# Optimization experiments

Hardware: AMD Instinct MI355X
Metric: run time of the kernel (lower is better)

The kernel has to match this reference:

```python
import jax, jax.numpy as jnp
import numpy as np

B, T, C, H = 4, 2048, 1024, 16
D = C // H  # head_dim = 64


def setup_inputs() -> dict:
    key = jax.random.key(0)
    ks = jax.random.split(key, 4)
    scale = 1.0 / np.sqrt(C)
    return {
        "x": jax.random.normal(ks[0], (B, T, C), dtype=jnp.float32),
        "attn_mask": jnp.ones((B, T), dtype=jnp.int32),
        "W_qkv": jax.random.normal(ks[1], (C, 3 * C), dtype=jnp.float32) * scale,
        "b_qkv": jnp.zeros((3 * C,), dtype=jnp.float32),
        "W_proj": jax.random.normal(ks[2], (C, C), dtype=jnp.float32) * scale,
        "b_proj": jnp.zeros((C,), dtype=jnp.float32),
    }


def reference(x, attn_mask, W_qkv, b_qkv, W_proj, b_proj):
    b, t, c = x.shape
    qkv = x @ W_qkv + b_qkv                      # (B,T,3C)
    q, k, v = jnp.split(qkv, 3, axis=-1)
    # b t (h d) -> b h t d
    q = q.reshape(b, t, H, D).transpose(0, 2, 1, 3)
    k = k.reshape(b, t, H, D).transpose(0, 2, 1, 3)
    v = v.reshape(b, t, H, D).transpose(0, 2, 1, 3)
    att = jnp.einsum("bhtd,bhsd->bhts", q, k) / jnp.sqrt(jnp.float32(D))
    causal = jnp.tril(jnp.ones((t, t), dtype=bool))[None, None]       # (1,1,T,T)
    pad = (attn_mask[:, None, None, :t] != 0)                         # (B,1,1,T)
    att = jnp.where(causal & pad, att, -jnp.inf)
    att = jax.nn.softmax(att, axis=-1)
    y = jnp.einsum("bhts,bhsd->bhtd", att, v)   # (B,H,T,D)
    y = y.transpose(0, 2, 1, 3).reshape(b, t, c)
    return y @ W_proj + b_proj
```

## Files before the change

### kernel.cpp

```cpp
#include <hip/hip_runtime.h>
#include <math.h>

#define B_ 4
#define T_ 2048
#define C_ 1024
#define H_ 16
#define D_ 64
#define M_ (B_*T_)
#define N1_ (3*C_)

typedef __attribute__((ext_vector_type(8))) short bf16x8;
typedef __attribute__((ext_vector_type(4))) short bf16x4;
typedef __attribute__((ext_vector_type(4))) float f32x4;
typedef __attribute__((ext_vector_type(16))) float f32x16;

__device__ __forceinline__ short f2bf(float f){
  union { float f; unsigned u; } v; v.f = f;
  unsigned r = (v.u + 0x7fffu + ((v.u >> 16) & 1u)) >> 16;
  return (short)r;
}

__device__ __forceinline__ unsigned cvtpk(float lo, float hi){
  unsigned r;
  asm("v_cvt_pk_bf16_f32 %0, %1, %2" : "=v"(r) : "v"(lo), "v"(hi));
  return r;
}

__device__ __forceinline__ void plswap(unsigned &a, unsigned &b){
  asm volatile("v_permlane32_swap_b32 %0, %1" : "+v"(a), "+v"(b));
}
__device__ __forceinline__ float xhalf_add(float x){
  unsigned a = __float_as_uint(x), b = a;
  asm volatile("v_permlane32_swap_b32 %0, %1" : "+v"(a), "+v"(b));
  return __uint_as_float(a) + __uint_as_float(b);
}

__device__ __forceinline__ void gll16(const void* g, void* l){
  __builtin_amdgcn_global_load_lds((const __attribute__((address_space(1))) void*)g,
                                   (__attribute__((address_space(3))) void*)l, 16, 0, 0);
}

__global__ __launch_bounds__(256) void convx(const float* __restrict__ x, short* __restrict__ xb, int n){
  int i = (blockIdx.x*256 + threadIdx.x)*8;
  if (i >= n) return;
  float4 a = *(const float4*)(x+i), b = *(const float4*)(x+i+4);
  bf16x8 o;
  o[0]=f2bf(a.x); o[1]=f2bf(a.y); o[2]=f2bf(a.z); o[3]=f2bf(a.w);
  o[4]=f2bf(b.x); o[5]=f2bf(b.y); o[6]=f2bf(b.z); o[7]=f2bf(b.w);
  *(bf16x8*)(xb+i) = o;
}

__global__ __launch_bounds__(256) void transw(const float* __restrict__ W, short* __restrict__ Wt, int K, int N){
  __shared__ float tl[64][72];
  int tid = threadIdx.x;
  int n0 = blockIdx.x*64, k0 = blockIdx.y*64;
  #pragma unroll
  for (int i=0;i<4;i++){
    int row = (tid>>4) + i*16;
    int col4 = (tid&15)*4;
    float4 v = *(const float4*)&W[(size_t)(k0+row)*N + n0 + col4];
    *(float4*)&tl[row][col4] = v;
  }
  __syncthreads();
  #pragma unroll
  for (int i=0;i<2;i++){
    int nr = (tid>>3) + i*32;
    int ch = tid&7;
    bf16x8 o;
    #pragma unroll
    for (int e=0;e<8;e++) o[e] = f2bf(tl[ch*8+e][nr]);
    *(bf16x8*)&Wt[(size_t)(n0+nr)*K + k0 + ch*8] = o;
  }
}

__global__ __launch_bounds__(512) void gemm256(const short* __restrict__ A, const short* __restrict__ Bt,
           const float* __restrict__ bias, short* __restrict__ outb, int M, int N, int K)
{
  __shared__ __attribute__((aligned(128))) char LDSC[131072];
  const int tid = threadIdx.x;
  const int wv = tid>>6, ln = tid&63;
  const int lnr = ln&15, lg = ln>>4;
  const int wm = wv>>2, wn = wv&3;
  const int nx = gridDim.x;
  const int nwg = nx*gridDim.y;
  const int lin = blockIdx.x + nx*blockIdx.y;
  const int swz = (lin&7)*(nwg>>3) + (lin>>3);
  const int m0 = (swz/nx)*256, n0 = (swz%nx)*256;

  const int sr = tid>>3;
  const int sg = (tid&7) ^ (sr&7);
  const short* Ag = A  + (size_t)(m0 + sr)*K + sg*8;
  const short* Bg = Bt + (size_t)(n0 + sr)*K + sg*8;
  const int wv8 = wv*1024;

  const int fsw = (lg ^ (lnr&7))<<4;
  const int aln = (wm*128 + lnr)*128 + fsw;
  const int bln = (wn*64  + lnr)*128 + fsw;

  auto STAGE = [&](int kt, int bi){
    const short* a = Ag + kt*64;
    const short* b = Bg + kt*64;
    char* ab = LDSC + bi*32768 + wv8;
    char* bb = LDSC + 65536 + bi*32768 + wv8;
    gll16(a,                 ab);
    gll16(a + (size_t)64*K,  ab + 8192);
    gll16(a + (size_t)128*K, ab + 16384);
    gll16(a + (size_t)192*K, ab + 24576);
    gll16(b,                 bb);
    gll16(b + (size_t)64*K,  bb + 8192);
    gll16(b + (size_t)128*K, bb + 16384);
    gll16(b + (size_t)192*K, bb + 24576);
  };

  f32x4 acc[8][4];
  #pragma unroll
  for (int i=0;i<8;i++)
    #pragma unroll
    for (int j=0;j<4;j++) acc[i][j] = (f32x4){0.f,0.f,0.f,0.f};

  const int NT = K >> 6;
  STAGE(0, 0);
  asm volatile("s_waitcnt vmcnt(0)" ::: "memory");
  __builtin_amdgcn_sched_barrier(0);
  __builtin_amdgcn_s_barrier();
  __builtin_amdgcn_sched_barrier(0);

  #pragma unroll 1
  for (int kt = 0; kt < NT; kt++){
    const int cb = kt & 1;
    if (kt + 1 < NT) STAGE(kt + 1, cb ^ 1);

    const char* ab = LDSC + cb*32768;
    const char* bb = LDSC + 65536 + cb*32768;
    #pragma unroll
    for (int ks=0; ks<2; ks++){
      bf16x8 af[8], bfr[4];
      #pragma unroll
      for (int mi=0;mi<8;mi++) af[mi]  = *(const bf16x8*)(ab + ((aln + mi*2048) ^ (ks<<6)));
      #pragma unroll
      for (int ni=0;ni<4;ni++) bfr[ni] = *(const bf16x8*)(bb + ((bln + ni*2048) ^ (ks<<6)));
      __builtin_amdgcn_s_setprio(1);
      #pragma unroll
      for (int mi=0;mi<8;mi++)
        #pragma unroll
        for (int ni=0;ni<4;ni++)
          acc[mi][ni] = __builtin_amdgcn_mfma_f32_16x16x32_bf16(af[mi], bfr[ni], acc[mi][ni], 0,0,0);
      __builtin_amdgcn_s_setprio(0);
    }

    __builtin_amdgcn_sched_barrier(0);
    asm volatile("s_waitcnt vmcnt(0)" ::: "memory");
    __builtin_amdgcn_sched_barrier(0);
    __builtin_amdgcn_s_barrier();
    __builtin_amdgcn_sched_barrier(0);
  }

  #pragma unroll
  for (int mi=0;mi<8;mi++){
    #pragma unroll
    for (int ni=0;ni<4;ni++){
      int col = n0 + wn*64 + ni*16 + lnr;
      float bv = bias[col];
      #pragma unroll
      for (int r=0;r<4;r++){
        int row = m0 + wm*128 + mi*16 + lg*4 + r;
        float v = acc[mi][ni][r] + bv;
        if (col < C_) v *= 0.18033688f;
        outb[(size_t)row*N + col] = f2bf(v);
      }
    }
  }
}

__global__ __launch_bounds__(512) void gemm_proj(const short* __restrict__ A, const short* __restrict__ Bt,
           const float* __restrict__ bias, float* __restrict__ outf, int M, int N, int K)
{
  __shared__ __attribute__((aligned(128))) char LDSC[147456];
  const int tid = threadIdx.x;
  const int wv = tid>>6, ln = tid&63;
  const int lnr = ln&15, lg = ln>>4;
  const int wm = wv>>1, wn = wv&1;
  const int nx = gridDim.x;
  const int nwg = nx*gridDim.y;
  const int lin = blockIdx.x + nx*blockIdx.y;
  const int swz = (lin&7)*(nwg>>3) + (lin>>3);
  const int m0 = (swz/nx)*256, n0 = (swz%nx)*128;

  const int srA = tid>>3;
  const int sg  = (tid&7) ^ (srA&7);
  const short* Ag = A  + (size_t)(m0 + srA)*K + sg*8;
  const short* Bg = Bt + (size_t)(n0 + srA)*K + sg*8;

  const int fsw = (lg ^ (lnr&7))<<4;
  const int aln = (wm*64 + lnr)*128 + fsw;
  const int bln = (wn*64 + lnr)*128 + fsw;

  auto STAGE = [&](int kt, int bi){
    const short* a = Ag + kt*64;
    const short* b = Bg + kt*64;
    char* ab = LDSC + bi*32768 + wv*1024;
    char* bb = LDSC + 98304 + bi*16384 + wv*1024;
    gll16(a,                ab);
    gll16(a + (size_t)64*K, ab + 8192);
    gll16(a + (size_t)128*K, ab + 16384);
    gll16(a + (size_t)192*K, ab + 24576);
    gll16(b,                bb);
    gll16(b + (size_t)64*K, bb + 8192);
  };

  f32x4 acc[4][4];
  #pragma unroll
  for (int i=0;i<4;i++)
    #pragma unroll
    for (int j=0;j<4;j++) acc[i][j] = (f32x4){0.f,0.f,0.f,0.f};

  const int NT = K >> 6;
  STAGE(0, 0);
  STAGE(1, 1);
  asm volatile("s_waitcnt vmcnt(6)" ::: "memory");
  __builtin_amdgcn_sched_barrier(0);
  __builtin_amdgcn_s_barrier();
  __builtin_amdgcn_sched_barrier(0);

  int cb = 0, sb = 2;
  #pragma unroll 1
  for (int kt = 0; kt < NT; kt++){
    if (kt + 2 < NT) STAGE(kt + 2, sb);

    const char* ab = LDSC + cb*32768;
    const char* bb = LDSC + 98304 + cb*16384;
    bf16x8 af[4][2], bfr[4][2];
    #pragma unroll
    for (int mi=0;mi<4;mi++)
      #pragma unroll
      for (int ks=0;ks<2;ks++)
        af[mi][ks] = *(const bf16x8*)(ab + ((aln + mi*2048) ^ (ks<<6)));
    #pragma unroll
    for (int ni=0;ni<4;ni++)
      #pragma unroll
      for (int ks=0;ks<2;ks++)
        bfr[ni][ks] = *(const bf16x8*)(bb + ((bln + ni*2048) ^ (ks<<6)));

    __builtin_amdgcn_s_setprio(1);
    #pragma unroll
    for (int mi=0;mi<4;mi++)
      #pragma unroll
      for (int ni=0;ni<4;ni++)
        #pragma unroll
        for (int ks=0;ks<2;ks++)
          acc[mi][ni] = __builtin_amdgcn_mfma_f32_16x16x32_bf16(af[mi][ks], bfr[ni][ks], acc[mi][ni], 0,0,0);
    __builtin_amdgcn_s_setprio(0);

    if (kt < NT-1){
      __builtin_amdgcn_sched_barrier(0);
      if (kt < NT-2){ asm volatile("s_waitcnt vmcnt(6)" ::: "memory"); }
      else          { asm volatile("s_waitcnt vmcnt(0)" ::: "memory"); }
      __builtin_amdgcn_sched_barrier(0);
      __builtin_amdgcn_s_barrier();
      __builtin_amdgcn_sched_barrier(0);
    }
    cb = (cb==2) ? 0 : cb+1;
    sb = (sb==2) ? 0 : sb+1;
  }

  #pragma unroll
  for (int mi=0;mi<4;mi++){
    #pragma unroll
    for (int ni=0;ni<4;ni++){
      int col = n0 + wn*64 + ni*16 + lnr;
      float bv = bias[col];
      #pragma unroll
      for (int r=0;r<4;r++){
        int row = m0 + wm*64 + mi*16 + lg*4 + r;
        outf[(size_t)row*N + col] = acc[mi][ni][r] + bv;
      }
    }
  }
}

__global__ __launch_bounds__(256) void transv(const short* __restrict__ qkv, short* __restrict__ vt){
  __shared__ short tl[64][72];
  int tid = threadIdx.x;
  int t0 = blockIdx.x*64, bh = blockIdx.y;
  int b = bh>>4, h = bh&15;
  int tr = tid>>2, cc = (tid&3)*16;
  const short* src = &qkv[(size_t)(b*T_ + t0 + tr)*N1_ + 2*C_ + h*D_ + cc];
  #pragma unroll
  for (int i=0;i<4;i++){
    bf16x4 v = *(const bf16x4*)(src + i*4);
    *(bf16x4*)&tl[tr][cc + i*4] = v;
  }
  __syncthreads();
  int d = tid>>2, tc = (tid&3)*16;
  #pragma unroll
  for (int i=0;i<2;i++){
    bf16x8 o;
    #pragma unroll
    for (int e=0;e<8;e++) o[e] = tl[tc + i*8 + e][d];
    *(bf16x8*)&vt[(size_t)(bh*D_ + d)*T_ + t0 + tc + i*8] = o;
  }
}

__global__ __launch_bounds__(256) void attn14(const short* __restrict__ qkv, const short* __restrict__ vt,
           const int* __restrict__ mask, short* __restrict__ yb)
{
  __shared__ short Ks[64*64];
  __shared__ short Vs[64*64];
  const int tid = threadIdx.x;
  const int wv = tid>>6, ln = tid&63;
  const int l31 = ln & 31, hi = ln >> 5;
  const int bh = blockIdx.x, b = bh>>4, hd = bh&15;
  const int c = 15 - (int)blockIdx.y;
  const float MC = 11.541561f;

  const int srow = tid>>3;
  const int scol = (tid&7) ^ (srow&7);
  const short* kgb = qkv + (size_t)(b*T_ + srow)*N1_ + C_ + hd*D_ + scol*8;
  const short* vgb = vt  + (size_t)((bh<<6) + srow)*T_ + scol*8;
  int fa[4];
  #pragma unroll
  for (int i=0;i<4;i++)
    fa[i] = l31*128 + ((((i<<1)+hi) ^ (l31&7)) << 4);

  char* ksb = (char*)Ks;
  char* vsb = (char*)Vs;

  const int q0w = c*128 + wv*32;
  const int ntb  = 2*c + 2;
  const int myNt = 2*c + 1 + (wv>>1);

  bf16x8 qf[4];
  const short* qbase = qkv + (size_t)(b*T_ + q0w + l31)*N1_ + hd*D_ + hi*8;
  #pragma unroll
  for (int ds=0; ds<4; ds++) qf[ds] = *(const bf16x8*)(qbase + ds*16);

  f32x16 o0, o1;
  #pragma unroll
  for (int r=0;r<16;r++){ o0[r]=0.f; o1[r]=0.f; }
  float lsum = 0.f;

  #pragma unroll 1
  for (int jt = 0; jt < ntb; jt++){
    const int j0 = jt << 6;

    int mval = mask[b*T_ + j0 + ln];
    const short* kg = kgb + (size_t)j0*N1_;
    const short* vg = vgb + j0;
    gll16(kg,                    ksb + wv*1024);
    gll16(kg + (size_t)32*N1_,   ksb + 4096 + wv*1024);
    gll16(vg,                    vsb + wv*1024);
    gll16(vg + (size_t)32*T_,    vsb + 4096 + wv*1024);
    unsigned long long bm = __ballot(mval != 0);
    __syncthreads();

    if (jt < myNt){
      f32x16 s0, s1;
      #pragma unroll
      for (int r=0;r<16;r++){ s0[r]=-MC; s1[r]=-MC; }
      __builtin_amdgcn_s_setprio(1);
      #pragma unroll
      for (int ds=0; ds<4; ds++){
        bf16x8 k0 = *(const bf16x8*)(ksb + fa[ds]);
        bf16x8 k1 = *(const bf16x8*)(ksb + fa[ds] + 4096);
        s0 = __builtin_amdgcn_mfma_f32_32x32x16_bf16(k0, qf[ds], s0, 0,0,0);
        s1 = __builtin_amdgcn_mfma_f32_32x32x16_bf16(k1, qf[ds], s1, 0,0,0);
      }
      __builtin_amdgcn_s_setprio(0);

      const int qglob = q0w + l31;
      const bool allm = (bm == ~0ull);
      if (!allm){
        #pragma unroll
        for (int r=0;r<16;r++){
          int kr = (r&3) + 8*(r>>2) + 4*hi;
          bool ok0 = (j0 + kr      <= qglob) && ((bm >> kr) & 1);
          bool ok1 = (j0 + kr + 32 <= qglob) && ((bm >> (kr+32)) & 1);
          s0[r] = ok0 ? s0[r] : -INFINITY;
          s1[r] = ok1 ? s1[r] : -INFINITY;
        }
      } else if (j0 + 63 > q0w){
        #pragma unroll
        for (int r=0;r<16;r++){
          int kr = (r&3) + 8*(r>>2) + 4*hi;
          s0[r] = (j0 + kr      <= qglob) ? s0[r] : -INFINITY;
          s1[r] = (j0 + kr + 32 <= qglob) ? s1[r] : -INFINITY;
        }
      }

      #pragma unroll
      for (int r=0;r<16;r++){
        s0[r] = __builtin_amdgcn_exp2f(s0[r]);
        s1[r] = __builtin_amdgcn_exp2f(s1[r]);
      }
      float u[8];
      #pragma unroll
      for (int i=0;i<8;i++) u[i] = (s0[i]+s0[i+8]) + (s1[i]+s1[i+8]);
      #pragma unroll
      for (int i=0;i<4;i++) u[i] = u[i] + u[i+4];
      float ps = (u[0]+u[1]) + (u[2]+u[3]);
      lsum += xhalf_add(ps);

      unsigned LA[2][4], LB[2][4];
      #pragma unroll
      for (int rq=0; rq<4; rq++){
        LA[0][rq] = cvtpk(s0[4*rq],   s0[4*rq+1]);
        LB[0][rq] = cvtpk(s0[4*rq+2], s0[4*rq+3]);
        LA[1][rq] = cvtpk(s1[4*rq],   s1[4*rq+1]);
        LB[1][rq] = cvtpk(s1[4*rq+2], s1[4*rq+3]);
      }

      #pragma unroll
      for (int kt2=0; kt2<4; kt2++){
        const int kt = kt2>>1, sub = kt2&1;
        bf16x8 v0 = *(const bf16x8*)(vsb + fa[kt2]);
        bf16x8 v1 = *(const bf16x8*)(vsb + fa[kt2] + 4096);
        unsigned a0 = LA[kt][2*sub], a1 = LA[kt][2*sub+1];
        unsigned b0 = LB[kt][2*sub], b1 = LB[kt][2*sub+1];
        plswap(a0, a1);
        plswap(b0, b1);
        union { unsigned u[4]; bf16x8 v; } pf;
        pf.u[0] = a0; pf.u[1] = b0; pf.u[2] = a1; pf.u[3] = b1;
        __builtin_amdgcn_s_setprio(1);
        o0 = __builtin_amdgcn_mfma_f32_32x32x16_bf16(pf.v, v0, o0, 0,0,0);
        o1 = __builtin_amdgcn_mfma_f32_32x32x16_bf16(pf.v, v1, o1, 0,0,0);
        __builtin_amdgcn_s_setprio(0);
      }
    }
    __syncthreads();
  }

  float linv = 1.0f / lsum;
  #pragma unroll
  for (int r=0;r<16;r++){
    int qs = (r&3) + 8*(r>>2) + 4*hi;
    float lv = __shfl(linv, qs);
    size_t base = (size_t)(b*T_ + q0w + qs)*C_ + hd*D_ + l31;
    yb[base]      = f2bf(o0[r]*lv);
    yb[base + 32] = f2bf(o1[r]*lv);
  }
}

extern "C" void kernel_launch(void* const* d_in, const int* in_sizes, int n_in,
                              void* d_out, int out_size, void* d_ws, size_t ws_size,
                              hipStream_t stream){
  const float* x     = (const float*)d_in[0];
  const int*   mask  = (const int*)d_in[1];
  const float* Wqkv  = (const float*)d_in[2];
  const float* bqkv  = (const float*)d_in[3];
  const float* Wproj = (const float*)d_in[4];
  const float* bproj = (const float*)d_in[5];
  float* out = (float*)d_out;

  char* w = (char*)d_ws;
  short* xb     = (short*)w; w += (size_t)M_*C_*2;
  short* wqkvT  = (short*)w; w += (size_t)N1_*C_*2;
  short* wprojT = (short*)w; w += (size_t)C_*C_*2;
  short* qkvb   = (short*)w; w += (size_t)M_*N1_*2;
  short* vtb    = (short*)w; w += (size_t)B_*H_*D_*T_*2;
  short* yb     = (short*)w; w += (size_t)M_*C_*2;

  convx<<<dim3((M_*C_)/(256*8)), 256, 0, stream>>>(x, xb, M_*C_);
  transw<<<dim3(N1_/64, C_/64), 256, 0, stream>>>(Wqkv, wqkvT, C_, N1_);
  transw<<<dim3(C_/64,  C_/64), 256, 0, stream>>>(Wproj, wprojT, C_, C_);
  gemm256<<<dim3(N1_/256, M_/256), 512, 0, stream>>>(xb, wqkvT, bqkv, qkvb, M_, N1_, C_);
  transv<<<dim3(T_/64, B_*H_), 256, 0, stream>>>(qkvb, vtb);
  attn14<<<dim3(B_*H_, 16), 256, 0, stream>>>(qkvb, vtb, mask, yb);
  gemm_proj<<<dim3(C_/128, M_/256), 512, 0, stream>>>(yb, wprojT, bproj, out, M_, C_, C_);
}
```

Before: 170.4 us.

## Split GEMM K-tile into half-stages with finer-grained vmcnt pipelining

```diff
diff --git a/kernel.cpp b/kernel.cpp
--- a/kernel.cpp
+++ b/kernel.cpp
@@ -80,36 +80,32 @@
   const int tid = threadIdx.x;
   const int wv = tid>>6, ln = tid&63;
   const int lnr = ln&15, lg = ln>>4;
-  const int wm = wv>>2, wn = wv&3;
+  const int wm = wv&1, wn = wv>>1;
   const int nx = gridDim.x;
   const int nwg = nx*gridDim.y;
   const int lin = blockIdx.x + nx*blockIdx.y;
   const int swz = (lin&7)*(nwg>>3) + (lin>>3);
   const int m0 = (swz/nx)*256, n0 = (swz%nx)*256;
 
-  const int sr = tid>>3;
-  const int sg = (tid&7) ^ (sr&7);
-  const short* Ag = A  + (size_t)(m0 + sr)*K + sg*8;
-  const short* Bg = Bt + (size_t)(n0 + sr)*K + sg*8;
-  const int wv8 = wv*1024;
-
-  const int fsw = (lg ^ (lnr&7))<<4;
-  const int aln = (wm*128 + lnr)*128 + fsw;
-  const int bln = (wn*64  + lnr)*128 + fsw;
-
-  auto STAGE = [&](int kt, int bi){
-    const short* a = Ag + kt*64;
-    const short* b = Bg + kt*64;
-    char* ab = LDSC + bi*32768 + wv8;
-    char* bb = LDSC + 65536 + bi*32768 + wv8;
+  const int srow = wv*16 + (ln>>2);
+  const int bsrc = (ln&3) ^ ((srow>>1)&3);
+  const short* aSrc = A  + (size_t)(m0 + srow)*K + bsrc*8;
+  const short* bSrc = Bt + (size_t)(n0 + srow)*K + bsrc*8;
+
+  const int fsw2 = (lg ^ ((lnr>>1)&3)) << 4;
+  const int aoff = (wm*128 + lnr)*64 + fsw2;
+  const int boff = (wn*64  + lnr)*64 + fsw2;
+
+  auto STAGE = [&](int kt, int s){
+    const int d = kt & 1;
+    char* ab = LDSC + d*65536 + s*16384 + wv*1024;
+    char* bb = LDSC + d*65536 + 32768 + s*16384 + wv*1024;
+    const short* a = aSrc + kt*64 + s*32;
+    const short* b = bSrc + kt*64 + s*32;
     gll16(a,                 ab);
-    gll16(a + (size_t)64*K,  ab + 8192);
-    gll16(a + (size_t)128*K, ab + 16384);
-    gll16(a + (size_t)192*K, ab + 24576);
+    gll16(a + (size_t)128*K, ab + 8192);
     gll16(b,                 bb);
-    gll16(b + (size_t)64*K,  bb + 8192);
-    gll16(b + (size_t)128*K, bb + 16384);
-    gll16(b + (size_t)192*K, bb + 24576);
+    gll16(b + (size_t)128*K, bb + 8192);
   };
 
   f32x4 acc[8][4];
@@ -120,25 +116,33 @@
 
   const int NT = K >> 6;
   STAGE(0, 0);
-  asm volatile("s_waitcnt vmcnt(0)" ::: "memory");
-  __builtin_amdgcn_sched_barrier(0);
-  __builtin_amdgcn_s_barrier();
-  __builtin_amdgcn_sched_barrier(0);
+  STAGE(0, 1);
 
   #pragma unroll 1
   for (int kt = 0; kt < NT; kt++){
-    const int cb = kt & 1;
-    if (kt + 1 < NT) STAGE(kt + 1, cb ^ 1);
-
-    const char* ab = LDSC + cb*32768;
-    const char* bb = LDSC + 65536 + cb*32768;
-    #pragma unroll
-    for (int ks=0; ks<2; ks++){
+    const char* bufA = LDSC + (kt&1)*65536;
+    const char* bufB = bufA + 32768;
+    #pragma unroll
+    for (int s = 0; s < 2; s++){
+      __builtin_amdgcn_sched_barrier(0);
+      if (kt == NT-1 && s == 1) { asm volatile("s_waitcnt vmcnt(0)" ::: "memory"); }
+      else                      { asm volatile("s_waitcnt vmcnt(4)" ::: "memory"); }
+      __builtin_amdgcn_sched_barrier(0);
+      __builtin_amdgcn_s_barrier();
+      __builtin_amdgcn_sched_barrier(0);
+
+      const char* ah = bufA + s*16384;
+      const char* bh = bufB + s*16384;
       bf16x8 af[8], bfr[4];
       #pragma unroll
-      for (int mi=0;mi<8;mi++) af[mi]  = *(const bf16x8*)(ab + ((aln + mi*2048) ^ (ks<<6)));
-      #pragma unroll
-      for (int ni=0;ni<4;ni++) bfr[ni] = *(const bf16x8*)(bb + ((bln + ni*2048) ^ (ks<<6)));
+      for (int mi=0;mi<8;mi++) af[mi]  = *(const bf16x8*)(ah + aoff + mi*1024);
+      #pragma unroll
+      for (int ni=0;ni<4;ni++) bfr[ni] = *(const bf16x8*)(bh + boff + ni*1024);
+
+      if (kt + 1 < NT) STAGE(kt + 1, s);
+
+      asm volatile("s_waitcnt lgkmcnt(0)" ::: "memory");
+      __builtin_amdgcn_sched_barrier(0);
       __builtin_amdgcn_s_setprio(1);
       #pragma unroll
       for (int mi=0;mi<8;mi++)
@@ -147,12 +151,6 @@
           acc[mi][ni] = __builtin_amdgcn_mfma_f32_16x16x32_bf16(af[mi], bfr[ni], acc[mi][ni], 0,0,0);
       __builtin_amdgcn_s_setprio(0);
     }
-
-    __builtin_amdgcn_sched_barrier(0);
-    asm volatile("s_waitcnt vmcnt(0)" ::: "memory");
-    __builtin_amdgcn_sched_barrier(0);
-    __builtin_amdgcn_s_barrier();
-    __builtin_amdgcn_sched_barrier(0);
   }
 
   #pragma unroll
```

Result: no change. 171.3 us (median of 4 runs) (+0.5%).
